# Kernel optimization log

Hardware: AMD Instinct MI355X
Metric: run time of the kernel (lower is better)

The kernel has to match this reference:

```python
import jax, jax.numpy as jnp
import numpy as np

B, S, D, H = 4, 2048, 1024, 16
DH = D // H


def setup_inputs() -> dict:
    key = jax.random.key(0)
    ks = jax.random.split(key, 5)
    scale = 0.02
    return {
        "in_features": jax.random.normal(ks[0], (B, S, D), dtype=jnp.float32),
        "Wq": jax.random.normal(ks[1], (D, D), dtype=jnp.float32) * scale,
        "Wk": jax.random.normal(ks[2], (D, D), dtype=jnp.float32) * scale,
        "Wv": jax.random.normal(ks[3], (D, D), dtype=jnp.float32) * scale,
        "Wo": jax.random.normal(ks[4], (D, D), dtype=jnp.float32) * scale,
    }


def reference(in_features, Wq, Wk, Wv, Wo):
    x = in_features  # [B, S, D]
    # projections: einsum '... s d_in, d_model d_in -> ... s d_model'  == x @ W.T
    q = jnp.einsum('bsd,md->bsm', x, Wq)
    k = jnp.einsum('bsd,md->bsm', x, Wk)
    v = jnp.einsum('bsd,md->bsm', x, Wv)
    # split heads: [B, H, S, DH]
    q = q.reshape(B, S, H, DH).transpose(0, 2, 1, 3)
    k = k.reshape(B, S, H, DH).transpose(0, 2, 1, 3)
    v = v.reshape(B, S, H, DH).transpose(0, 2, 1, 3)
    scale = 1.0 / jnp.sqrt(jnp.asarray(DH, dtype=q.dtype))
    scores = jnp.einsum('bhqd,bhkd->bhqk', q, k) * scale  # [B, H, S, S]
    causal = jnp.tril(jnp.ones((S, S), dtype=bool))
    scores = jnp.where(causal[None, None, :, :], scores, -jnp.inf)
    attn = jax.nn.softmax(scores, axis=-1)
    out = jnp.einsum('bhqk,bhkd->bhqd', attn, v)  # [B, H, S, DH]
    out = out.transpose(0, 2, 1, 3).reshape(B, S, D)
    # output projection: einsum '... s d_v, d_model d_v -> ... s d_model' == out @ Wo.T
    return jnp.einsum('bsd,md->bsm', out, Wo)
```

## Files before the change

### kernel.cpp

```cpp
#include <hip/hip_runtime.h>

typedef unsigned short u16;
typedef unsigned int u32;
typedef __attribute__((ext_vector_type(8))) short bf16x8;
typedef __attribute__((ext_vector_type(4))) short bf16x4;
typedef __attribute__((ext_vector_type(4))) float f32x4;

#define S_LEN 2048
#define NHEAD 16
#define DHEAD 64
#define DMODEL 1024

__device__ __forceinline__ u16 f2bf(float f) {
  unsigned u = __builtin_bit_cast(unsigned, f);
  unsigned r = (u + 0x7fffu + ((u >> 16) & 1u)) >> 16;
  return (u16)r;
}

__device__ __forceinline__ void gld_lds16(const void* g, void* l) {
  __builtin_amdgcn_global_load_lds((const __attribute__((address_space(1))) unsigned*)g,
                                   (__attribute__((address_space(3))) unsigned*)l,
                                   16, 0, 0);
}

__global__ void cast_bf16_kernel(const float* __restrict__ in, u16* __restrict__ out, int n4) {
  int i = blockIdx.x * 256 + threadIdx.x;
  if (i >= n4) return;
  float4 v = reinterpret_cast<const float4*>(in)[i];
  ushort4 o;
  o.x = f2bf(v.x); o.y = f2bf(v.y); o.z = f2bf(v.z); o.w = f2bf(v.w);
  reinterpret_cast<ushort4*>(out)[i] = o;
}

__global__ void cast_w_kernel(const float* __restrict__ Wq, const float* __restrict__ Wk,
                              const float* __restrict__ Wv, const float* __restrict__ Wo,
                              u16* __restrict__ out) {
  int id = blockIdx.x * 256 + threadIdx.x;
  int wsel = id >> 18, j = id & 262143;
  const float* s = wsel < 2 ? (wsel == 0 ? Wq : Wk) : (wsel == 2 ? Wv : Wo);
  float4 v = reinterpret_cast<const float4*>(s)[j];
  ushort4 o;
  o.x = f2bf(v.x); o.y = f2bf(v.y); o.z = f2bf(v.z); o.w = f2bf(v.w);
  reinterpret_cast<ushort4*>(out)[id] = o;
}

#define MFMA_Q(mlo, nlo)                                                                     \
  _Pragma("unroll") for (int m_ = 0; m_ < 2; ++m_)                                           \
  _Pragma("unroll") for (int n_ = 0; n_ < 3; ++n_)                                           \
  _Pragma("unroll") for (int kk_ = 0; kk_ < 2; ++kk_)                                        \
    acc[(mlo) + m_][(nlo) + n_] = __builtin_amdgcn_mfma_f32_16x16x32_bf16(                   \
        af[(mlo) + m_][kk_], bf[(nlo) + n_][kk_], acc[(mlo) + m_][(nlo) + n_], 0, 0, 0);

#define VM5 do { __builtin_amdgcn_sched_barrier(0);                                          \
  asm volatile("s_waitcnt vmcnt(5)" ::: "memory");                                           \
  __builtin_amdgcn_sched_barrier(0); } while (0)
#define VM0 do { __builtin_amdgcn_sched_barrier(0);                                          \
  asm volatile("s_waitcnt vmcnt(0)" ::: "memory");                                           \
  __builtin_amdgcn_sched_barrier(0); } while (0)

#define HALF_ITER(bb, e, WAIT) do {                                                          \
  const u16* aW = aW0 + (bb)*28672;                                                          \
  const u16* bW = bW0 + (bb)*28672;                                                          \
                              \
  _Pragma("unroll") for (int m_ = 0; m_ < 2; ++m_) {                                         \
    af[m_][0] = rdA(aW, m_, 0); af[m_][1] = rdA(aW, m_, 1); }                                \
  _Pragma("unroll") for (int n_ = 0; n_ < 3; ++n_) {                                         \
    bf[n_][0] = rdB(bW, n_, 0); bf[n_][1] = rdB(bW, n_, 1); }                                \
  stgB((e) + 1, 1); stgB((e) + 1, 2);                                                        \
  __builtin_amdgcn_s_barrier();                                                              \
  __builtin_amdgcn_s_setprio(1); MFMA_Q(0, 0) __builtin_amdgcn_s_setprio(0);                 \
  __builtin_amdgcn_s_barrier();                                                              \
                                                                       \
  _Pragma("unroll") for (int m_ = 0; m_ < 2; ++m_) {                                         \
    af[2 + m_][0] = rdA(aW, 2 + m_, 0); af[2 + m_][1] = rdA(aW, 2 + m_, 1); }                \
  __builtin_amdgcn_s_barrier();                                                              \
  __builtin_amdgcn_s_setprio(1); MFMA_Q(2, 0) __builtin_amdgcn_s_setprio(0);                 \
  __builtin_amdgcn_s_barrier();                                                              \
                         \
  _Pragma("unroll") for (int n_ = 0; n_ < 3; ++n_) {                                         \
    bf[3 + n_][0] = rdB(bW, 3 + n_, 0); bf[3 + n_][1] = rdB(bW, 3 + n_, 1); }                \
  stgA((e) + 2, 0); stgA((e) + 2, 1);                                                        \
  __builtin_amdgcn_s_barrier();                                                              \
  __builtin_amdgcn_s_setprio(1); MFMA_Q(0, 3) __builtin_amdgcn_s_setprio(0);                 \
  __builtin_amdgcn_s_barrier();                                                              \
                                          \
  stgB((e) + 2, 0);                                                                          \
  __builtin_amdgcn_s_barrier();                                                              \
  __builtin_amdgcn_s_setprio(1); MFMA_Q(2, 3) __builtin_amdgcn_s_setprio(0);                 \
  WAIT;                                                                                      \
  __builtin_amdgcn_s_barrier();                                                              \
} while (0)

__global__ __launch_bounds__(512, 2) void gemm_qkv(const u16* __restrict__ A,
                                                   const u16* __restrict__ Bw,
                                                   u16* __restrict__ Qb) {
  __shared__ u16 lds[57344];
  const int bid = blockIdx.x;
  const int xcd = bid & 7, v = bid >> 3;
  const int by = xcd * 4 + (v & 3), bx = v >> 2;
  const int brow = by * 256, bcol = bx * 192;
  const int tid = threadIdx.x;
  const int w = tid >> 6, lane = tid & 63;
  const int wm = w >> 1, wn = w & 1;
  const int c = lane & 15, qr = lane >> 4;
  const int sqz = (qr ^ (c & 7)) * 8;

  auto stgA = [&](int tau, int half) {
    if (tau >= 16) return;
    u16* region = lds + (tau & 1) * 28672 + half * 8192;
    int rowb = brow + half * 128;
    int k0 = tau * 64;
#pragma unroll
    for (int i = 0; i < 2; ++i) {
      int slot = i * 512 + tid;
      int r = slot >> 3, cb = slot & 7;
      int cbs = cb ^ (r & 7);
      gld_lds16(A + (size_t)(rowb + r) * DMODEL + k0 + cbs * 8, region + (i * 512 + w * 64) * 8);
    }
  };
  auto stgB = [&](int tau, int third) {
    if (tau >= 16) return;
    u16* region = lds + (tau & 1) * 28672 + 16384 + third * 4096;
    int rowb = bcol + third * 64;
    int k0 = tau * 64;
    int r = tid >> 3, cb = tid & 7;
    int cbs = cb ^ (r & 7);
    gld_lds16(Bw + (size_t)(rowb + r) * DMODEL + k0 + cbs * 8, region + (w * 64) * 8);
  };

  auto rdA = [&](const u16* base, int m, int kk) {
    return *(const bf16x8*)(base + (m * 16 + c) * 64 + (sqz ^ (kk << 5)));
  };
  auto rdB = [&](const u16* base, int n, int kk) {
    return *(const bf16x8*)(base + (n * 16 + c) * 64 + (sqz ^ (kk << 5)));
  };

  f32x4 acc[4][6];
#pragma unroll
  for (int m = 0; m < 4; ++m)
#pragma unroll
    for (int n = 0; n < 6; ++n) acc[m][n] = (f32x4){0.f, 0.f, 0.f, 0.f};
  bf16x8 af[4][2], bf[6][2];
  const u16* aW0 = lds + wm * 4096;
  const u16* bW0 = lds + 16384 + wn * 6144;

  stgA(0, 0); stgA(0, 1); stgB(0, 0); stgB(0, 1); stgB(0, 2);
  stgA(1, 0); stgA(1, 1); stgB(1, 0);
  VM5;
  __builtin_amdgcn_s_barrier();

#pragma unroll 1
  for (int t = 0; t < 8; ++t) {
    const int e = 2 * t;
    HALF_ITER(0, e, if (t < 7) { VM5; } else { VM0; });
    HALF_ITER(1, e + 1, if (t < 7) { VM5; });
  }

  u16* Kb = Qb + 8388608;
  u16* Vt = Kb + 8388608;
#pragma unroll
  for (int m = 0; m < 4; ++m) {
#pragma unroll
    for (int n = 0; n < 6; ++n) {
      f32x4 a = acc[m][n];
      int gm0 = brow + wm * 64 + m * 16 + qr * 4;
      int gn = bcol + wn * 96 + n * 16 + c;
      int mat = gn >> 10, gl = gn & 1023;
      int hh = gl >> 6, dh = gl & 63;
      int b = gm0 >> 11;
      if (mat == 2) {
        int s0 = gm0 & 2047;
        ushort4 pk;
        pk.x = f2bf(a[0]); pk.y = f2bf(a[1]); pk.z = f2bf(a[2]); pk.w = f2bf(a[3]);
        *reinterpret_cast<ushort4*>(Vt + ((size_t)(b * NHEAD + hh) * DHEAD + dh) * S_LEN + s0) = pk;
      } else {
        float scale = (mat == 0) ? 0.1803368801111204f : 1.0f;
        u16* dst = (mat == 0) ? Qb : Kb;
#pragma unroll
        for (int r = 0; r < 4; ++r) {
          int gm = gm0 + r;
          int s = gm & 2047;
          dst[((size_t)(b * NHEAD + hh) * S_LEN + s) * DHEAD + dh] = f2bf(a[r] * scale);
        }
      }
    }
  }
}

__global__ __launch_bounds__(256) void gemm_bt(const u16* __restrict__ A, const u16* __restrict__ Bw,
                                               float* __restrict__ outp) {
  __shared__ u16 lA[2][128 * 32];
  __shared__ u16 lB[2][128 * 32];
  const int hw = blockIdx.x;
  const int xcd = hw & 7, vv = hw >> 3;
  const int bx = vv >> 3, by = xcd * 8 + (vv & 7);
  const int tid = threadIdx.x;
  const int w = tid >> 6, lane = tid & 63;
  const int wm = w >> 1, wn = w & 1;
  const int c = lane & 15, qr = lane >> 4;
  const int brow = by * 128, bcol = bx * 128;
  f32x4 acc[4][4];
#pragma unroll
  for (int m = 0; m < 4; ++m)
#pragma unroll
    for (int n = 0; n < 4; ++n) acc[m][n] = (f32x4){0.f, 0.f, 0.f, 0.f};

  auto stage = [&](int kt, int bsel) {
    const int k0 = kt * 32;
#pragma unroll
    for (int i = 0; i < 2; ++i) {
      int slot = i * 256 + w * 64 + lane;
      int r = slot >> 2, sg = slot & 3;
      gld_lds16(A + (size_t)(brow + r) * DMODEL + k0 + sg * 8, &lA[bsel][(i * 256 + w * 64) * 8]);
      gld_lds16(Bw + (size_t)(bcol + r) * DMODEL + k0 + sg * 8, &lB[bsel][(i * 256 + w * 64) * 8]);
    }
  };

  stage(0, 0);
  __syncthreads();
  int cur = 0;
  for (int kt = 0; kt < 32; ++kt) {
    if (kt < 31) stage(kt + 1, cur ^ 1);
    bf16x8 af[4], bfr[4];
#pragma unroll
    for (int m = 0; m < 4; ++m) af[m] = *(const bf16x8*)(&lA[cur][(wm * 64 + m * 16 + c) * 32 + qr * 8]);
#pragma unroll
    for (int n = 0; n < 4; ++n) bfr[n] = *(const bf16x8*)(&lB[cur][(wn * 64 + n * 16 + c) * 32 + qr * 8]);
    __builtin_amdgcn_s_setprio(1);
#pragma unroll
    for (int m = 0; m < 4; ++m)
#pragma unroll
      for (int n = 0; n < 4; ++n)
        acc[m][n] = __builtin_amdgcn_mfma_f32_16x16x32_bf16(af[m], bfr[n], acc[m][n], 0, 0, 0);
    __builtin_amdgcn_s_setprio(0);
    __syncthreads();
    cur ^= 1;
  }

  const int rb = qr * 4;
#pragma unroll
  for (int m = 0; m < 4; ++m)
#pragma unroll
    for (int n = 0; n < 4; ++n) {
      f32x4 a = acc[m][n];
      int gm0 = brow + wm * 64 + m * 16 + rb;
      int gn = bcol + wn * 64 + n * 16 + c;
#pragma unroll
      for (int r = 0; r < 4; ++r) outp[(size_t)(gm0 + r) * DMODEL + gn] = a[r];
    }
}

__global__ __launch_bounds__(512, 4) void attn_kernel(const u16* __restrict__ Q, const u16* __restrict__ K,
                                                      const u16* __restrict__ Vt, u16* __restrict__ O) {
  __shared__ u16 lsK[2][64 * 64];
  __shared__ u16 lsV[2][64 * 64];
  __shared__ u16 lsP[8][16 * 64];
  const int hw = blockIdx.x;
  const int xcd = hw & 7, vv = hw >> 3;
  const int by = xcd * 8 + (vv >> 3);
  const int j = vv & 7;
  const int tid = threadIdx.x;
  const int w = tid >> 6, lane = tid & 63;
  const int c = lane & 15, qr = lane >> 4;
  const int b = by >> 4, h = by & 15;
  u16* lp = lsP[w];

  const int q0A = j * 128 + w * 16;
  const int q0B = (15 - j) * 128 + w * 16;
  const int ndA = q0A >> 6, ndB = q0B >> 6;
  const int ntiles = 32 - 2 * j;

  const u16* qra = Q + ((size_t)by * S_LEN + q0A + c) * DHEAD;
  const u16* qrb = Q + ((size_t)by * S_LEN + q0B + c) * DHEAD;
  const bf16x8 aQA0 = *(const bf16x8*)(qra + qr * 8);
  const bf16x8 aQA1 = *(const bf16x8*)(qra + 32 + qr * 8);
  const bf16x8 aQB0 = *(const bf16x8*)(qrb + qr * 8);
  const bf16x8 aQB1 = *(const bf16x8*)(qrb + 32 + qr * 8);

  f32x4 oA[4], oB[4];
#pragma unroll
  for (int d = 0; d < 4; ++d) { oA[d] = (f32x4){0.f, 0.f, 0.f, 0.f}; oB[d] = oA[d]; }
  float mA = -1e30f, lA_ = 0.f, mB = -1e30f, lB_ = 0.f;

  auto stage = [&](int kt, int bsel) {
    const int kv0 = kt * 64;
    int r = tid >> 3, p = tid & 7;
    int ps = p ^ (r & 7);
    gld_lds16(K + ((size_t)by * S_LEN + kv0 + r) * DHEAD + ps * 8, &lsK[bsel][(w * 64) * 8]);
    gld_lds16(Vt + ((size_t)by * DHEAD + r) * S_LEN + kv0 + ps * 8, &lsV[bsel][(w * 64) * 8]);
  };

  auto process = [&](const u16* bK, const u16* bV, int kt, int nd, int q0,
                     const bf16x8& aQ0, const bf16x8& aQ1,
                     f32x4* o_acc, float& m_run, float& l_run) {
    const int kv0 = kt * 64;
    f32x4 sc[4];
    __builtin_amdgcn_s_setprio(1);
#pragma unroll
    for (int nt = 0; nt < 4; ++nt) {
      int row = nt * 16 + c;
      const bf16x8 k0 = *(const bf16x8*)(bK + row * 64 + ((qr ^ (row & 7)) * 8));
      const bf16x8 k1 = *(const bf16x8*)(bK + row * 64 + (((4 + qr) ^ (row & 7)) * 8));
      f32x4 z = (f32x4){0.f, 0.f, 0.f, 0.f};
      z = __builtin_amdgcn_mfma_f32_16x16x32_bf16(k0, aQ0, z, 0, 0, 0);
      z = __builtin_amdgcn_mfma_f32_16x16x32_bf16(k1, aQ1, z, 0, 0, 0);
      sc[nt] = z;
    }
    __builtin_amdgcn_s_setprio(0);

    if (kt == nd) {
#pragma unroll
      for (int nt = 0; nt < 4; ++nt)
#pragma unroll
        for (int r = 0; r < 4; ++r) {
          int k_g = kv0 + nt * 16 + qr * 4 + r;
          int q_g = q0 + c;
          if (k_g > q_g) sc[nt][r] = -1e30f;
        }
    }

    float tm = fmaxf(fmaxf(fmaxf(sc[0][0], sc[0][1]), fmaxf(sc[0][2], sc[0][3])),
                     fmaxf(fmaxf(sc[1][0], sc[1][1]), fmaxf(sc[1][2], sc[1][3])));
    tm = fmaxf(tm, fmaxf(fmaxf(fmaxf(sc[2][0], sc[2][1]), fmaxf(sc[2][2], sc[2][3])),
                         fmaxf(fmaxf(sc[3][0], sc[3][1]), fmaxf(sc[3][2], sc[3][3]))));
    tm = fmaxf(tm, __shfl_xor(tm, 16));
    tm = fmaxf(tm, __shfl_xor(tm, 32));
    if (tm > m_run + 11.5f) {
      float al = __builtin_amdgcn_exp2f(m_run - tm);
      l_run *= al;
#pragma unroll
      for (int dt = 0; dt < 4; ++dt)
#pragma unroll
        for (int r = 0; r < 4; ++r) o_acc[dt][r] *= al;
      m_run = tm;
    }
    float rs = 0.f;
#pragma unroll
    for (int nt = 0; nt < 4; ++nt) {
      float p0 = __builtin_amdgcn_exp2f(sc[nt][0] - m_run);
      float p1 = __builtin_amdgcn_exp2f(sc[nt][1] - m_run);
      float p2 = __builtin_amdgcn_exp2f(sc[nt][2] - m_run);
      float p3 = __builtin_amdgcn_exp2f(sc[nt][3] - m_run);
      rs += (p0 + p1) + (p2 + p3);
      u32 w01 = __builtin_amdgcn_perm(__builtin_bit_cast(u32, p1), __builtin_bit_cast(u32, p0), 0x07060302u);
      u32 w23 = __builtin_amdgcn_perm(__builtin_bit_cast(u32, p3), __builtin_bit_cast(u32, p2), 0x07060302u);
      uint2 pk; pk.x = w01; pk.y = w23;
      *reinterpret_cast<uint2*>(lp + c * 64 + (((nt * 4 + qr) ^ c) * 4)) = pk;
    }
    rs += __shfl_xor(rs, 16);
    rs += __shfl_xor(rs, 32);
    l_run += rs;

    bf16x8 pb[2];
#pragma unroll
    for (int ks = 0; ks < 2; ++ks) {
      bf16x4 lo = *(const bf16x4*)(lp + c * 64 + (((ks * 8 + qr * 2) ^ c) * 4));
      bf16x4 hi = *(const bf16x4*)(lp + c * 64 + (((ks * 8 + qr * 2 + 1) ^ c) * 4));
      pb[ks] = (bf16x8){lo[0], lo[1], lo[2], lo[3], hi[0], hi[1], hi[2], hi[3]};
    }
    __builtin_amdgcn_s_setprio(1);
#pragma unroll
    for (int dt = 0; dt < 4; ++dt) {
      int rowv = dt * 16 + c;
#pragma unroll
      for (int ks = 0; ks < 2; ++ks) {
        const bf16x8 vb = *(const bf16x8*)(bV + rowv * 64 + (((ks * 4 + qr) ^ (rowv & 7)) * 8));
        o_acc[dt] = __builtin_amdgcn_mfma_f32_16x16x32_bf16(vb, pb[ks], o_acc[dt], 0, 0, 0);
      }
    }
    __builtin_amdgcn_s_setprio(0);
  };

  stage(0, 0);
  __syncthreads();
  for (int kt = 0; kt < ntiles; kt += 2) {
    if (kt + 1 < ntiles) stage(kt + 1, 1);
    if (kt <= ndB) process(lsK[0], lsV[0], kt, ndB, q0B, aQB0, aQB1, oB, mB, lB_);
    if (kt <= ndA) process(lsK[0], lsV[0], kt, ndA, q0A, aQA0, aQA1, oA, mA, lA_);
    __syncthreads();
    const int k2 = kt + 1;
    if (k2 + 1 < ntiles) stage(k2 + 1, 0);
    if (k2 <= ndB) process(lsK[1], lsV[1], k2, ndB, q0B, aQB0, aQB1, oB, mB, lB_);
    if (k2 <= ndA) process(lsK[1], lsV[1], k2, ndA, q0A, aQA0, aQA1, oA, mA, lA_);
    __syncthreads();
  }

  {
    float rl = 1.0f / lB_;
    int s = q0B + c;
#pragma unroll
    for (int dt = 0; dt < 4; ++dt) {
      ushort4 ok;
#pragma unroll
      for (int r = 0; r < 4; ++r) ((u16*)&ok)[r] = f2bf(oB[dt][r] * rl);
      *reinterpret_cast<ushort4*>(O + (((size_t)b * S_LEN + s) * NHEAD + h) * DHEAD + dt * 16 + qr * 4) = ok;
    }
  }
  {
    float rl = 1.0f / lA_;
    int s = q0A + c;
#pragma unroll
    for (int dt = 0; dt < 4; ++dt) {
      ushort4 ok;
#pragma unroll
      for (int r = 0; r < 4; ++r) ((u16*)&ok)[r] = f2bf(oA[dt][r] * rl);
      *reinterpret_cast<ushort4*>(O + (((size_t)b * S_LEN + s) * NHEAD + h) * DHEAD + dt * 16 + qr * 4) = ok;
    }
  }
}

extern "C" void kernel_launch(void* const* d_in, const int* in_sizes, int n_in,
                              void* d_out, int out_size, void* d_ws, size_t ws_size,
                              hipStream_t stream) {
  (void)in_sizes; (void)n_in; (void)out_size; (void)ws_size;
  const float* x  = (const float*)d_in[0];
  const float* Wq = (const float*)d_in[1];
  const float* Wk = (const float*)d_in[2];
  const float* Wv = (const float*)d_in[3];
  const float* Wo = (const float*)d_in[4];

  u16* ws  = (u16*)d_ws;
  u16* xb  = ws;
  u16* wqb = xb  + 8388608;
  u16* wob = wqb + 3145728;
  u16* Qb  = wqb + 4194304;
  u16* Kb  = Qb  + 8388608;
  u16* Vt  = Kb  + 8388608;
  u16* Ob  = Vt  + 8388608;

  cast_bf16_kernel<<<8192, 256, 0, stream>>>(x, xb, 2097152);
  cast_w_kernel<<<4096, 256, 0, stream>>>(Wq, Wk, Wv, Wo, wqb);

  gemm_qkv<<<512, 512, 0, stream>>>(xb, wqb, Qb);
  attn_kernel<<<512, 512, 0, stream>>>(Qb, Kb, Vt, Ob);
  gemm_bt<<<512, 256, 0, stream>>>(Ob, wob, (float*)d_out);
}
```

Measured before the change: 173.8 us.

## Restructure causal attention to 32-row query tiles per wave with K/V reuse

The attention kernel moves from 512-thread blocks that pair a low and a high query block (load balancing) to 256-thread blocks. Each block now covers one 128-row query block, and each wave handles 32 query rows (two 16-row subtiles), so every K/V fragment read from LDS feeds two MFMAs. The P scratch buffer switches from XOR swizzling to a padded 72-element stride, and the grid doubles to 1024 blocks ordered longest-first. This drops the balanced pairing, so per-block work now varies with query position and the scheduler must absorb that imbalance. Register pressure per wave also rises.

```diff
diff --git a/kernel.cpp b/kernel.cpp
--- a/kernel.cpp
+++ b/kernel.cpp
@@ -61,7 +61,6 @@
 #define HALF_ITER(bb, e, WAIT) do {                                                          \
   const u16* aW = aW0 + (bb)*28672;                                                          \
   const u16* bW = bW0 + (bb)*28672;                                                          \
-                              \
   _Pragma("unroll") for (int m_ = 0; m_ < 2; ++m_) {                                         \
     af[m_][0] = rdA(aW, m_, 0); af[m_][1] = rdA(aW, m_, 1); }                                \
   _Pragma("unroll") for (int n_ = 0; n_ < 3; ++n_) {                                         \
@@ -70,20 +69,17 @@
   __builtin_amdgcn_s_barrier();                                                              \
   __builtin_amdgcn_s_setprio(1); MFMA_Q(0, 0) __builtin_amdgcn_s_setprio(0);                 \
   __builtin_amdgcn_s_barrier();                                                              \
-                                                                       \
   _Pragma("unroll") for (int m_ = 0; m_ < 2; ++m_) {                                         \
     af[2 + m_][0] = rdA(aW, 2 + m_, 0); af[2 + m_][1] = rdA(aW, 2 + m_, 1); }                \
   __builtin_amdgcn_s_barrier();                                                              \
   __builtin_amdgcn_s_setprio(1); MFMA_Q(2, 0) __builtin_amdgcn_s_setprio(0);                 \
   __builtin_amdgcn_s_barrier();                                                              \
-                         \
   _Pragma("unroll") for (int n_ = 0; n_ < 3; ++n_) {                                         \
     bf[3 + n_][0] = rdB(bW, 3 + n_, 0); bf[3 + n_][1] = rdB(bW, 3 + n_, 1); }                \
   stgA((e) + 2, 0); stgA((e) + 2, 1);                                                        \
   __builtin_amdgcn_s_barrier();                                                              \
   __builtin_amdgcn_s_setprio(1); MFMA_Q(0, 3) __builtin_amdgcn_s_setprio(0);                 \
   __builtin_amdgcn_s_barrier();                                                              \
-                                          \
   stgB((e) + 2, 0);                                                                          \
   __builtin_amdgcn_s_barrier();                                                              \
   __builtin_amdgcn_s_setprio(1); MFMA_Q(2, 3) __builtin_amdgcn_s_setprio(0);                 \
@@ -250,122 +246,136 @@
     }
 }
 
-__global__ __launch_bounds__(512, 4) void attn_kernel(const u16* __restrict__ Q, const u16* __restrict__ K,
+__global__ __launch_bounds__(256, 3) void attn_kernel(const u16* __restrict__ Q, const u16* __restrict__ K,
                                                       const u16* __restrict__ Vt, u16* __restrict__ O) {
   __shared__ u16 lsK[2][64 * 64];
   __shared__ u16 lsV[2][64 * 64];
-  __shared__ u16 lsP[8][16 * 64];
-  const int hw = blockIdx.x;
-  const int xcd = hw & 7, vv = hw >> 3;
-  const int by = xcd * 8 + (vv >> 3);
-  const int j = vv & 7;
+  __shared__ u16 lsP[4][32 * 72];
+  const int x = blockIdx.x;
+  const int xcd = x & 7, v = x >> 3;
+  const int by = xcd * 8 + (v >> 4);
+  const int g = 15 - (v & 15);
   const int tid = threadIdx.x;
   const int w = tid >> 6, lane = tid & 63;
   const int c = lane & 15, qr = lane >> 4;
   const int b = by >> 4, h = by & 15;
   u16* lp = lsP[w];
 
-  const int q0A = j * 128 + w * 16;
-  const int q0B = (15 - j) * 128 + w * 16;
-  const int ndA = q0A >> 6, ndB = q0B >> 6;
-  const int ntiles = 32 - 2 * j;
-
-  const u16* qra = Q + ((size_t)by * S_LEN + q0A + c) * DHEAD;
-  const u16* qrb = Q + ((size_t)by * S_LEN + q0B + c) * DHEAD;
-  const bf16x8 aQA0 = *(const bf16x8*)(qra + qr * 8);
-  const bf16x8 aQA1 = *(const bf16x8*)(qra + 32 + qr * 8);
-  const bf16x8 aQB0 = *(const bf16x8*)(qrb + qr * 8);
-  const bf16x8 aQB1 = *(const bf16x8*)(qrb + 32 + qr * 8);
-
-  f32x4 oA[4], oB[4];
-#pragma unroll
-  for (int d = 0; d < 4; ++d) { oA[d] = (f32x4){0.f, 0.f, 0.f, 0.f}; oB[d] = oA[d]; }
-  float mA = -1e30f, lA_ = 0.f, mB = -1e30f, lB_ = 0.f;
+  const int q0 = g * 128 + w * 32;
+  const int nd = 2 * g + (w >> 1);
+  const int ntiles = 2 * g + 2;
+
+  bf16x8 aQ[2][2];
+#pragma unroll
+  for (int qt = 0; qt < 2; ++qt)
+#pragma unroll
+    for (int ks = 0; ks < 2; ++ks)
+      aQ[qt][ks] = *(const bf16x8*)(Q + ((size_t)by * S_LEN + q0 + qt * 16 + c) * DHEAD + ks * 32 + qr * 8);
+
+  f32x4 o_acc[2][4];
+#pragma unroll
+  for (int qt = 0; qt < 2; ++qt)
+#pragma unroll
+    for (int d = 0; d < 4; ++d) o_acc[qt][d] = (f32x4){0.f, 0.f, 0.f, 0.f};
+  float m_run[2] = {-1e30f, -1e30f}, l_run[2] = {0.f, 0.f};
 
   auto stage = [&](int kt, int bsel) {
     const int kv0 = kt * 64;
-    int r = tid >> 3, p = tid & 7;
-    int ps = p ^ (r & 7);
-    gld_lds16(K + ((size_t)by * S_LEN + kv0 + r) * DHEAD + ps * 8, &lsK[bsel][(w * 64) * 8]);
-    gld_lds16(Vt + ((size_t)by * DHEAD + r) * S_LEN + kv0 + ps * 8, &lsV[bsel][(w * 64) * 8]);
-  };
-
-  auto process = [&](const u16* bK, const u16* bV, int kt, int nd, int q0,
-                     const bf16x8& aQ0, const bf16x8& aQ1,
-                     f32x4* o_acc, float& m_run, float& l_run) {
+#pragma unroll
+    for (int i = 0; i < 2; ++i) {
+      int s = i * 256 + tid;
+      int r = s >> 3, cb = s & 7;
+      int cbs = cb ^ (r & 7);
+      gld_lds16(K + ((size_t)by * S_LEN + kv0 + r) * DHEAD + cbs * 8, &lsK[bsel][(i * 256 + w * 64) * 8]);
+      gld_lds16(Vt + ((size_t)by * DHEAD + r) * S_LEN + kv0 + cbs * 8, &lsV[bsel][(i * 256 + w * 64) * 8]);
+    }
+  };
+
+  auto process = [&](const u16* bK, const u16* bV, int kt) {
     const int kv0 = kt * 64;
-    f32x4 sc[4];
+    f32x4 sc2[2][4];
     __builtin_amdgcn_s_setprio(1);
 #pragma unroll
     for (int nt = 0; nt < 4; ++nt) {
       int row = nt * 16 + c;
       const bf16x8 k0 = *(const bf16x8*)(bK + row * 64 + ((qr ^ (row & 7)) * 8));
       const bf16x8 k1 = *(const bf16x8*)(bK + row * 64 + (((4 + qr) ^ (row & 7)) * 8));
-      f32x4 z = (f32x4){0.f, 0.f, 0.f, 0.f};
-      z = __builtin_amdgcn_mfma_f32_16x16x32_bf16(k0, aQ0, z, 0, 0, 0);
-      z = __builtin_amdgcn_mfma_f32_16x16x32_bf16(k1, aQ1, z, 0, 0, 0);
-      sc[nt] = z;
+#pragma unroll
+      for (int qt = 0; qt < 2; ++qt) {
+        f32x4 z = (f32x4){0.f, 0.f, 0.f, 0.f};
+        z = __builtin_amdgcn_mfma_f32_16x16x32_bf16(k0, aQ[qt][0], z, 0, 0, 0);
+        z = __builtin_amdgcn_mfma_f32_16x16x32_bf16(k1, aQ[qt][1], z, 0, 0, 0);
+        sc2[qt][nt] = z;
+      }
     }
     __builtin_amdgcn_s_setprio(0);
 
     if (kt == nd) {
 #pragma unroll
-      for (int nt = 0; nt < 4; ++nt)
-#pragma unroll
-        for (int r = 0; r < 4; ++r) {
-          int k_g = kv0 + nt * 16 + qr * 4 + r;
-          int q_g = q0 + c;
-          if (k_g > q_g) sc[nt][r] = -1e30f;
-        }
-    }
-
-    float tm = fmaxf(fmaxf(fmaxf(sc[0][0], sc[0][1]), fmaxf(sc[0][2], sc[0][3])),
-                     fmaxf(fmaxf(sc[1][0], sc[1][1]), fmaxf(sc[1][2], sc[1][3])));
-    tm = fmaxf(tm, fmaxf(fmaxf(fmaxf(sc[2][0], sc[2][1]), fmaxf(sc[2][2], sc[2][3])),
-                         fmaxf(fmaxf(sc[3][0], sc[3][1]), fmaxf(sc[3][2], sc[3][3]))));
-    tm = fmaxf(tm, __shfl_xor(tm, 16));
-    tm = fmaxf(tm, __shfl_xor(tm, 32));
-    if (tm > m_run + 11.5f) {
-      float al = __builtin_amdgcn_exp2f(m_run - tm);
-      l_run *= al;
-#pragma unroll
-      for (int dt = 0; dt < 4; ++dt)
-#pragma unroll
-        for (int r = 0; r < 4; ++r) o_acc[dt][r] *= al;
-      m_run = tm;
-    }
-    float rs = 0.f;
-#pragma unroll
-    for (int nt = 0; nt < 4; ++nt) {
-      float p0 = __builtin_amdgcn_exp2f(sc[nt][0] - m_run);
-      float p1 = __builtin_amdgcn_exp2f(sc[nt][1] - m_run);
-      float p2 = __builtin_amdgcn_exp2f(sc[nt][2] - m_run);
-      float p3 = __builtin_amdgcn_exp2f(sc[nt][3] - m_run);
-      rs += (p0 + p1) + (p2 + p3);
-      u32 w01 = __builtin_amdgcn_perm(__builtin_bit_cast(u32, p1), __builtin_bit_cast(u32, p0), 0x07060302u);
-      u32 w23 = __builtin_amdgcn_perm(__builtin_bit_cast(u32, p3), __builtin_bit_cast(u32, p2), 0x07060302u);
-      uint2 pk; pk.x = w01; pk.y = w23;
-      *reinterpret_cast<uint2*>(lp + c * 64 + (((nt * 4 + qr) ^ c) * 4)) = pk;
-    }
-    rs += __shfl_xor(rs, 16);
-    rs += __shfl_xor(rs, 32);
-    l_run += rs;
-
-    bf16x8 pb[2];
-#pragma unroll
-    for (int ks = 0; ks < 2; ++ks) {
-      bf16x4 lo = *(const bf16x4*)(lp + c * 64 + (((ks * 8 + qr * 2) ^ c) * 4));
-      bf16x4 hi = *(const bf16x4*)(lp + c * 64 + (((ks * 8 + qr * 2 + 1) ^ c) * 4));
-      pb[ks] = (bf16x8){lo[0], lo[1], lo[2], lo[3], hi[0], hi[1], hi[2], hi[3]};
-    }
+      for (int qt = 0; qt < 2; ++qt)
+#pragma unroll
+        for (int nt = 0; nt < 4; ++nt)
+#pragma unroll
+          for (int r = 0; r < 4; ++r) {
+            int k_g = kv0 + nt * 16 + qr * 4 + r;
+            int q_g = q0 + qt * 16 + c;
+            if (k_g > q_g) sc2[qt][nt][r] = -1e30f;
+          }
+    }
+
+#pragma unroll
+    for (int qt = 0; qt < 2; ++qt) {
+      f32x4* sc = sc2[qt];
+      float tm = fmaxf(fmaxf(fmaxf(sc[0][0], sc[0][1]), fmaxf(sc[0][2], sc[0][3])),
+                       fmaxf(fmaxf(sc[1][0], sc[1][1]), fmaxf(sc[1][2], sc[1][3])));
+      tm = fmaxf(tm, fmaxf(fmaxf(fmaxf(sc[2][0], sc[2][1]), fmaxf(sc[2][2], sc[2][3])),
+                           fmaxf(fmaxf(sc[3][0], sc[3][1]), fmaxf(sc[3][2], sc[3][3]))));
+      tm = fmaxf(tm, __shfl_xor(tm, 16));
+      tm = fmaxf(tm, __shfl_xor(tm, 32));
+      if (tm > m_run[qt] + 11.5f) {
+        float al = __builtin_amdgcn_exp2f(m_run[qt] - tm);
+        l_run[qt] *= al;
+#pragma unroll
+        for (int dt = 0; dt < 4; ++dt)
+#pragma unroll
+          for (int r = 0; r < 4; ++r) o_acc[qt][dt][r] *= al;
+        m_run[qt] = tm;
+      }
+      float rs = 0.f;
+#pragma unroll
+      for (int nt = 0; nt < 4; ++nt) {
+        float p0 = __builtin_amdgcn_exp2f(sc[nt][0] - m_run[qt]);
+        float p1 = __builtin_amdgcn_exp2f(sc[nt][1] - m_run[qt]);
+        float p2 = __builtin_amdgcn_exp2f(sc[nt][2] - m_run[qt]);
+        float p3 = __builtin_amdgcn_exp2f(sc[nt][3] - m_run[qt]);
+        rs += (p0 + p1) + (p2 + p3);
+        u32 w01 = __builtin_amdgcn_perm(__builtin_bit_cast(u32, p1), __builtin_bit_cast(u32, p0), 0x07060302u);
+        u32 w23 = __builtin_amdgcn_perm(__builtin_bit_cast(u32, p3), __builtin_bit_cast(u32, p2), 0x07060302u);
+        uint2 pk; pk.x = w01; pk.y = w23;
+        *reinterpret_cast<uint2*>(lp + (qt * 16 + c) * 72 + (nt * 4 + qr) * 4) = pk;
+      }
+      rs += __shfl_xor(rs, 16);
+      rs += __shfl_xor(rs, 32);
+      l_run[qt] += rs;
+    }
+
+    bf16x8 pb[2][2];
+#pragma unroll
+    for (int qt = 0; qt < 2; ++qt)
+#pragma unroll
+      for (int ks = 0; ks < 2; ++ks)
+        pb[qt][ks] = *(const bf16x8*)(lp + (qt * 16 + c) * 72 + (ks * 8 + qr * 2) * 4);
+
     __builtin_amdgcn_s_setprio(1);
 #pragma unroll
     for (int dt = 0; dt < 4; ++dt) {
       int rowv = dt * 16 + c;
-#pragma unroll
-      for (int ks = 0; ks < 2; ++ks) {
-        const bf16x8 vb = *(const bf16x8*)(bV + rowv * 64 + (((ks * 4 + qr) ^ (rowv & 7)) * 8));
-        o_acc[dt] = __builtin_amdgcn_mfma_f32_16x16x32_bf16(vb, pb[ks], o_acc[dt], 0, 0, 0);
+      const bf16x8 v0 = *(const bf16x8*)(bV + rowv * 64 + ((qr ^ (rowv & 7)) * 8));
+      const bf16x8 v1 = *(const bf16x8*)(bV + rowv * 64 + (((4 + qr) ^ (rowv & 7)) * 8));
+#pragma unroll
+      for (int qt = 0; qt < 2; ++qt) {
+        o_acc[qt][dt] = __builtin_amdgcn_mfma_f32_16x16x32_bf16(v0, pb[qt][0], o_acc[qt][dt], 0, 0, 0);
+        o_acc[qt][dt] = __builtin_amdgcn_mfma_f32_16x16x32_bf16(v1, pb[qt][1], o_acc[qt][dt], 0, 0, 0);
       }
     }
     __builtin_amdgcn_s_setprio(0);
@@ -375,35 +385,22 @@
   __syncthreads();
   for (int kt = 0; kt < ntiles; kt += 2) {
     if (kt + 1 < ntiles) stage(kt + 1, 1);
-    if (kt <= ndB) process(lsK[0], lsV[0], kt, ndB, q0B, aQB0, aQB1, oB, mB, lB_);
-    if (kt <= ndA) process(lsK[0], lsV[0], kt, ndA, q0A, aQA0, aQA1, oA, mA, lA_);
+    if (kt <= nd) process(lsK[0], lsV[0], kt);
     __syncthreads();
-    const int k2 = kt + 1;
-    if (k2 + 1 < ntiles) stage(k2 + 1, 0);
-    if (k2 <= ndB) process(lsK[1], lsV[1], k2, ndB, q0B, aQB0, aQB1, oB, mB, lB_);
-    if (k2 <= ndA) process(lsK[1], lsV[1], k2, ndA, q0A, aQA0, aQA1, oA, mA, lA_);
+    if (kt + 2 < ntiles) stage(kt + 2, 0);
+    if (kt + 1 <= nd) process(lsK[1], lsV[1], kt + 1);
     __syncthreads();
   }
 
-  {
-    float rl = 1.0f / lB_;
-    int s = q0B + c;
+#pragma unroll
+  for (int qt = 0; qt < 2; ++qt) {
+    float rl = 1.0f / l_run[qt];
+    int s = q0 + qt * 16 + c;
 #pragma unroll
     for (int dt = 0; dt < 4; ++dt) {
       ushort4 ok;
 #pragma unroll
-      for (int r = 0; r < 4; ++r) ((u16*)&ok)[r] = f2bf(oB[dt][r] * rl);
-      *reinterpret_cast<ushort4*>(O + (((size_t)b * S_LEN + s) * NHEAD + h) * DHEAD + dt * 16 + qr * 4) = ok;
-    }
-  }
-  {
-    float rl = 1.0f / lA_;
-    int s = q0A + c;
-#pragma unroll
-    for (int dt = 0; dt < 4; ++dt) {
-      ushort4 ok;
-#pragma unroll
-      for (int r = 0; r < 4; ++r) ((u16*)&ok)[r] = f2bf(oA[dt][r] * rl);
+      for (int r = 0; r < 4; ++r) ((u16*)&ok)[r] = f2bf(o_acc[qt][dt][r] * rl);
       *reinterpret_cast<ushort4*>(O + (((size_t)b * S_LEN + s) * NHEAD + h) * DHEAD + dt * 16 + qr * 4) = ok;
     }
   }
@@ -432,6 +429,6 @@
   cast_w_kernel<<<4096, 256, 0, stream>>>(Wq, Wk, Wv, Wo, wqb);
 
   gemm_qkv<<<512, 512, 0, stream>>>(xb, wqb, Qb);
-  attn_kernel<<<512, 512, 0, stream>>>(Qb, Kb, Vt, Ob);
+  attn_kernel<<<1024, 256, 0, stream>>>(Qb, Kb, Vt, Ob);
   gemm_bt<<<512, 256, 0, stream>>>(Ob, wob, (float*)d_out);
 }
```

New measurement: 194.0 us. 11.6% more time.

## Split paired-query attention blocks into one tile per block and fuse cast kernels

Applied to the files above, without the earlier changes.

The attention kernel no longer has each block handle a complementary pair of query tiles (j and 15-j) for causal load balance. It now launches 1024 blocks, each handling a single 128-row query tile, with heavier tiles scheduled first via g = 15 - (v>>3). This halves per-block register state and lets the scheduler balance the causal work, but it gives up the explicit pairing and reloads K/V tiles for every query tile. Separately, the x and weight fp32-to-bf16 casts are merged into one launch to save a kernel launch.

```diff
diff --git a/kernel.cpp b/kernel.cpp
--- a/kernel.cpp
+++ b/kernel.cpp
@@ -23,21 +23,21 @@
                                    16, 0, 0);
 }
 
-__global__ void cast_bf16_kernel(const float* __restrict__ in, u16* __restrict__ out, int n4) {
-  int i = blockIdx.x * 256 + threadIdx.x;
-  if (i >= n4) return;
-  float4 v = reinterpret_cast<const float4*>(in)[i];
-  ushort4 o;
-  o.x = f2bf(v.x); o.y = f2bf(v.y); o.z = f2bf(v.z); o.w = f2bf(v.w);
-  reinterpret_cast<ushort4*>(out)[i] = o;
-}
-
-__global__ void cast_w_kernel(const float* __restrict__ Wq, const float* __restrict__ Wk,
-                              const float* __restrict__ Wv, const float* __restrict__ Wo,
-                              u16* __restrict__ out) {
+__global__ void cast_all_kernel(const float* __restrict__ x,
+                                const float* __restrict__ Wq, const float* __restrict__ Wk,
+                                const float* __restrict__ Wv, const float* __restrict__ Wo,
+                                u16* __restrict__ out) {
   int id = blockIdx.x * 256 + threadIdx.x;
-  int wsel = id >> 18, j = id & 262143;
-  const float* s = wsel < 2 ? (wsel == 0 ? Wq : Wk) : (wsel == 2 ? Wv : Wo);
+  const float* s;
+  int j;
+  if (id < 2097152) {
+    s = x; j = id;
+  } else {
+    int wid = id - 2097152;
+    int wsel = wid >> 18;
+    j = wid & 262143;
+    s = wsel < 2 ? (wsel == 0 ? Wq : Wk) : (wsel == 2 ? Wv : Wo);
+  }
   float4 v = reinterpret_cast<const float4*>(s)[j];
   ushort4 o;
   o.x = f2bf(v.x); o.y = f2bf(v.y); o.z = f2bf(v.z); o.w = f2bf(v.w);
@@ -61,7 +61,6 @@
 #define HALF_ITER(bb, e, WAIT) do {                                                          \
   const u16* aW = aW0 + (bb)*28672;                                                          \
   const u16* bW = bW0 + (bb)*28672;                                                          \
-                              \
   _Pragma("unroll") for (int m_ = 0; m_ < 2; ++m_) {                                         \
     af[m_][0] = rdA(aW, m_, 0); af[m_][1] = rdA(aW, m_, 1); }                                \
   _Pragma("unroll") for (int n_ = 0; n_ < 3; ++n_) {                                         \
@@ -70,20 +69,17 @@
   __builtin_amdgcn_s_barrier();                                                              \
   __builtin_amdgcn_s_setprio(1); MFMA_Q(0, 0) __builtin_amdgcn_s_setprio(0);                 \
   __builtin_amdgcn_s_barrier();                                                              \
-                                                                       \
   _Pragma("unroll") for (int m_ = 0; m_ < 2; ++m_) {                                         \
     af[2 + m_][0] = rdA(aW, 2 + m_, 0); af[2 + m_][1] = rdA(aW, 2 + m_, 1); }                \
   __builtin_amdgcn_s_barrier();                                                              \
   __builtin_amdgcn_s_setprio(1); MFMA_Q(2, 0) __builtin_amdgcn_s_setprio(0);                 \
   __builtin_amdgcn_s_barrier();                                                              \
-                         \
   _Pragma("unroll") for (int n_ = 0; n_ < 3; ++n_) {                                         \
     bf[3 + n_][0] = rdB(bW, 3 + n_, 0); bf[3 + n_][1] = rdB(bW, 3 + n_, 1); }                \
-  stgA((e) + 2, 0); stgA((e) + 2, 1);                                                        \
+  stgA((e) + 2, 0); stgA((e) + 2, 1);                                                       \
   __builtin_amdgcn_s_barrier();                                                              \
   __builtin_amdgcn_s_setprio(1); MFMA_Q(0, 3) __builtin_amdgcn_s_setprio(0);                 \
   __builtin_amdgcn_s_barrier();                                                              \
-                                          \
   stgB((e) + 2, 0);                                                                          \
   __builtin_amdgcn_s_barrier();                                                              \
   __builtin_amdgcn_s_setprio(1); MFMA_Q(2, 3) __builtin_amdgcn_s_setprio(0);                 \
@@ -255,32 +251,28 @@
   __shared__ u16 lsK[2][64 * 64];
   __shared__ u16 lsV[2][64 * 64];
   __shared__ u16 lsP[8][16 * 64];
-  const int hw = blockIdx.x;
-  const int xcd = hw & 7, vv = hw >> 3;
-  const int by = xcd * 8 + (vv >> 3);
-  const int j = vv & 7;
+  const int x = blockIdx.x;
+  const int xcd = x & 7, v = x >> 3;
+  const int by = xcd * 8 + (v & 7);
+  const int g = 15 - (v >> 3);
   const int tid = threadIdx.x;
   const int w = tid >> 6, lane = tid & 63;
   const int c = lane & 15, qr = lane >> 4;
   const int b = by >> 4, h = by & 15;
   u16* lp = lsP[w];
 
-  const int q0A = j * 128 + w * 16;
-  const int q0B = (15 - j) * 128 + w * 16;
-  const int ndA = q0A >> 6, ndB = q0B >> 6;
-  const int ntiles = 32 - 2 * j;
-
-  const u16* qra = Q + ((size_t)by * S_LEN + q0A + c) * DHEAD;
-  const u16* qrb = Q + ((size_t)by * S_LEN + q0B + c) * DHEAD;
-  const bf16x8 aQA0 = *(const bf16x8*)(qra + qr * 8);
-  const bf16x8 aQA1 = *(const bf16x8*)(qra + 32 + qr * 8);
-  const bf16x8 aQB0 = *(const bf16x8*)(qrb + qr * 8);
-  const bf16x8 aQB1 = *(const bf16x8*)(qrb + 32 + qr * 8);
-
-  f32x4 oA[4], oB[4];
-#pragma unroll
-  for (int d = 0; d < 4; ++d) { oA[d] = (f32x4){0.f, 0.f, 0.f, 0.f}; oB[d] = oA[d]; }
-  float mA = -1e30f, lA_ = 0.f, mB = -1e30f, lB_ = 0.f;
+  const int q0 = g * 128 + w * 16;
+  const int nd = 2 * g + (w >> 2);
+  const int ntiles = 2 * g + 2;
+
+  const u16* qrow = Q + ((size_t)by * S_LEN + q0 + c) * DHEAD;
+  const bf16x8 aQ0 = *(const bf16x8*)(qrow + qr * 8);
+  const bf16x8 aQ1 = *(const bf16x8*)(qrow + 32 + qr * 8);
+
+  f32x4 o_acc[4];
+#pragma unroll
+  for (int d = 0; d < 4; ++d) o_acc[d] = (f32x4){0.f, 0.f, 0.f, 0.f};
+  float m_run = -1e30f, l_run = 0.f;
 
   auto stage = [&](int kt, int bsel) {
     const int kv0 = kt * 64;
@@ -290,9 +282,7 @@
     gld_lds16(Vt + ((size_t)by * DHEAD + r) * S_LEN + kv0 + ps * 8, &lsV[bsel][(w * 64) * 8]);
   };
 
-  auto process = [&](const u16* bK, const u16* bV, int kt, int nd, int q0,
-                     const bf16x8& aQ0, const bf16x8& aQ1,
-                     f32x4* o_acc, float& m_run, float& l_run) {
+  auto process = [&](const u16* bK, const u16* bV, int kt) {
     const int kv0 = kt * 64;
     f32x4 sc[4];
     __builtin_amdgcn_s_setprio(1);
@@ -375,35 +365,21 @@
   __syncthreads();
   for (int kt = 0; kt < ntiles; kt += 2) {
     if (kt + 1 < ntiles) stage(kt + 1, 1);
-    if (kt <= ndB) process(lsK[0], lsV[0], kt, ndB, q0B, aQB0, aQB1, oB, mB, lB_);
-    if (kt <= ndA) process(lsK[0], lsV[0], kt, ndA, q0A, aQA0, aQA1, oA, mA, lA_);
+    if (kt <= nd) process(lsK[0], lsV[0], kt);
     __syncthreads();
-    const int k2 = kt + 1;
-    if (k2 + 1 < ntiles) stage(k2 + 1, 0);
-    if (k2 <= ndB) process(lsK[1], lsV[1], k2, ndB, q0B, aQB0, aQB1, oB, mB, lB_);
-    if (k2 <= ndA) process(lsK[1], lsV[1], k2, ndA, q0A, aQA0, aQA1, oA, mA, lA_);
+    if (kt + 2 < ntiles) stage(kt + 2, 0);
+    if (kt + 1 <= nd) process(lsK[1], lsV[1], kt + 1);
     __syncthreads();
   }
 
   {
-    float rl = 1.0f / lB_;
-    int s = q0B + c;
+    float rl = 1.0f / l_run;
+    int s = q0 + c;
 #pragma unroll
     for (int dt = 0; dt < 4; ++dt) {
       ushort4 ok;
 #pragma unroll
-      for (int r = 0; r < 4; ++r) ((u16*)&ok)[r] = f2bf(oB[dt][r] * rl);
-      *reinterpret_cast<ushort4*>(O + (((size_t)b * S_LEN + s) * NHEAD + h) * DHEAD + dt * 16 + qr * 4) = ok;
-    }
-  }
-  {
-    float rl = 1.0f / lA_;
-    int s = q0A + c;
-#pragma unroll
-    for (int dt = 0; dt < 4; ++dt) {
-      ushort4 ok;
-#pragma unroll
-      for (int r = 0; r < 4; ++r) ((u16*)&ok)[r] = f2bf(oA[dt][r] * rl);
+      for (int r = 0; r < 4; ++r) ((u16*)&ok)[r] = f2bf(o_acc[dt][r] * rl);
       *reinterpret_cast<ushort4*>(O + (((size_t)b * S_LEN + s) * NHEAD + h) * DHEAD + dt * 16 + qr * 4) = ok;
     }
   }
@@ -428,10 +404,9 @@
   u16* Vt  = Kb  + 8388608;
   u16* Ob  = Vt  + 8388608;
 
-  cast_bf16_kernel<<<8192, 256, 0, stream>>>(x, xb, 2097152);
-  cast_w_kernel<<<4096, 256, 0, stream>>>(Wq, Wk, Wv, Wo, wqb);
+  cast_all_kernel<<<12288, 256, 0, stream>>>(x, Wq, Wk, Wv, Wo, xb);
 
   gemm_qkv<<<512, 512, 0, stream>>>(xb, wqb, Qb);
-  attn_kernel<<<512, 512, 0, stream>>>(Qb, Kb, Vt, Ob);
+  attn_kernel<<<1024, 512, 0, stream>>>(Qb, Kb, Vt, Ob);
   gemm_bt<<<512, 256, 0, stream>>>(Ob, wob, (float*)d_out);
 }
```

After: 171.5 us. No clear change (-1.3%).
